# Kernel tuning notes

Measured on AMD Instinct MI355X. Metric: run time of the kernel, lower is better.

## Reference

```python
import jax, jax.numpy as jnp
import numpy as np

BETA = 0.25
SK_EPSILONS = [0.0, 0.0, 0.003]
SK_ITERS = 50
B_SIZE = 262144
LATENT_DIM = 32
K = 256


def setup_inputs() -> dict:
    key = jax.random.key(0)
    kz, k0, k1, k2 = jax.random.split(key, 4)
    return {
        "z": jax.random.normal(kz, (B_SIZE, LATENT_DIM), dtype=jnp.float32),
        "cb0": jax.random.normal(k0, (K, LATENT_DIM), dtype=jnp.float32),
        "cb1": jax.random.normal(k1, (K, LATENT_DIM), dtype=jnp.float32),
        "cb2": jax.random.normal(k2, (K, LATENT_DIM), dtype=jnp.float32),
    }


def _sq_dists(residual, codebook):
    # ||r - c||^2 = ||r||^2 + ||c||^2 - 2 r.c  -> (B, K), avoids (B,K,D) broadcast
    r2 = jnp.sum(residual * residual, axis=1, keepdims=True)      # (B,1)
    c2 = jnp.sum(codebook * codebook, axis=1)                     # (K,)
    cross = residual @ codebook.T                                 # (B,K)
    return r2 + c2 - 2.0 * cross


def _sinkhorn(d_centered, epsilon, n_iters):
    # log-domain Sinkhorn-Knopp, matches torch reference
    B, Kk = d_centered.shape
    log_B = jnp.log(jnp.asarray(B, dtype=d_centered.dtype))
    log_K = jnp.log(jnp.asarray(Kk, dtype=d_centered.dtype))
    log_Q = -d_centered / epsilon
    log_Q = log_Q - jax.scipy.special.logsumexp(log_Q)

    def body(_, lq):
        lq = lq - jax.scipy.special.logsumexp(lq, axis=1, keepdims=True) - log_B
        lq = lq - jax.scipy.special.logsumexp(lq, axis=0, keepdims=True) - log_K
        return lq

    log_Q = jax.lax.fori_loop(0, n_iters, body, log_Q)
    return jnp.exp(log_Q + log_B)


def _quantize_level(residual, codebook, sk_epsilon, use_sk=True):
    dists = _sq_dists(residual, codebook)  # (B, K)
    codes_argmin = jnp.argmin(dists, axis=-1)
    if use_sk and sk_epsilon > 0:
        d = jax.lax.stop_gradient(dists)
        d_max = jnp.max(d)
        d_min = jnp.min(d)
        mid = (d_max + d_min) / 2
        amp = jnp.maximum(d_max - mid, 1e-05)
        Q = _sinkhorn((d - mid) / amp, sk_epsilon, SK_ITERS)
        bad = jnp.any(jnp.isnan(Q)) | jnp.any(jnp.isinf(Q))
        codes = jnp.where(bad, codes_argmin, jnp.argmax(Q, axis=-1))
    else:
        codes = codes_argmin
    quantized = codebook[codes]  # (B, D) gather
    return codes, quantized


def reference(z, cb0, cb1, cb2):
    codebooks = [cb0, cb1, cb2]
    sg = jax.lax.stop_gradient
    residual = z
    all_codes = []
    quantized_total = jnp.zeros_like(z)
    rq_loss = jnp.asarray(0.0, dtype=z.dtype)
    for codebook, sk_epsilon in zip(codebooks, SK_EPSILONS):
        codes, e = _quantize_level(residual, codebook, sk_epsilon, use_sk=True)
        all_codes.append(codes)
        rq_loss = rq_loss + jnp.mean((sg(residual) - e) ** 2)
        rq_loss = rq_loss + BETA * jnp.mean((residual - sg(e)) ** 2)
        e_st = residual + sg(e - residual)  # straight-through
        quantized_total = quantized_total + e_st
        residual = residual - sg(e)
    return (all_codes[0], all_codes[1], all_codes[2], quantized_total, rq_loss)
```

## Files before the change

### kernel.cpp

```cpp
#include <hip/hip_runtime.h>


#define BSZ   262144
#define DIM   32
#define KK    256
#define CHUNK 128
#define NBLK  (BSZ / CHUNK)
#define NIBLK (BSZ / 256)
#define LROW  36
#define SKEPS 0.003f
#define NIT   50

#define WS_SSQ  0
#define WS_MINK 1
#define WS_MAXK 2
#define WS_TWOT 3
#define WS_W0   256
#define WS_WA   512
#define WS_C2   1024
#define WSB_SIG 8192
#define WSB_BH  32768
#define WSB_BL  49152
#define WSB_QB  65536

#define OC0   0
#define OC1   BSZ
#define OC2   (2 * BSZ)
#define OQ    (3 * BSZ)
#define OLOSS (3 * BSZ + BSZ * DIM)
#define OU_AH (3u * BSZ)
#define OU_AL (3u * BSZ + 4194304u)

typedef short short8 __attribute__((ext_vector_type(8)));
typedef _Float16 half8 __attribute__((ext_vector_type(8)));
typedef float f32x4 __attribute__((ext_vector_type(4)));

#if __has_builtin(__builtin_amdgcn_exp2f)
#define EXP2(x) __builtin_amdgcn_exp2f(x)
#else
#define EXP2(x) exp2f(x)
#endif

#if __has_builtin(__builtin_amdgcn_update_dpp)
#define ROR16(x, N)                                                            \
  __int_as_float(__builtin_amdgcn_update_dpp(__float_as_int(x),                \
                 __float_as_int(x), 0x120 + (N), 0xF, 0xF, false))
#define ROR16I(x, N) __builtin_amdgcn_update_dpp((x), (x), 0x120 + (N), 0xF, 0xF, false)
#else
#define ROR16(x, N) __shfl_xor((x), (N))
#define ROR16I(x, N) __shfl_xor((x), (N))
#endif

__device__ __forceinline__ float wred_sum(float x) {
  x += ROR16(x, 1); x += ROR16(x, 2); x += ROR16(x, 4); x += ROR16(x, 8);
  x += __shfl_xor(x, 16); x += __shfl_xor(x, 32);
  return x;
}
__device__ __forceinline__ float wred_max(float x) {
  x = fmaxf(x, ROR16(x, 1)); x = fmaxf(x, ROR16(x, 2));
  x = fmaxf(x, ROR16(x, 4)); x = fmaxf(x, ROR16(x, 8));
  x = fmaxf(x, __shfl_xor(x, 16)); x = fmaxf(x, __shfl_xor(x, 32));
  return x;
}
__device__ __forceinline__ float wred_min(float x) {
  x = fminf(x, ROR16(x, 1)); x = fminf(x, ROR16(x, 2));
  x = fminf(x, ROR16(x, 4)); x = fminf(x, ROR16(x, 8));
  x = fminf(x, __shfl_xor(x, 16)); x = fminf(x, __shfl_xor(x, 32));
  return x;
}
__device__ __forceinline__ float g16_max(float x) {
  x = fmaxf(x, ROR16(x, 1)); x = fmaxf(x, ROR16(x, 2));
  x = fmaxf(x, ROR16(x, 4)); x = fmaxf(x, ROR16(x, 8));
  return x;
}
__device__ __forceinline__ float g16_sum(float x) {
  x += ROR16(x, 1); x += ROR16(x, 2); x += ROR16(x, 4); x += ROR16(x, 8);
  return x;
}
__device__ __forceinline__ void g16_argmax(float& v, int& j) {
  { float ov = ROR16(v,1); int oj = ROR16I(j,1); if (ov > v || (ov == v && oj < j)) { v = ov; j = oj; } }
  { float ov = ROR16(v,2); int oj = ROR16I(j,2); if (ov > v || (ov == v && oj < j)) { v = ov; j = oj; } }
  { float ov = ROR16(v,4); int oj = ROR16I(j,4); if (ov > v || (ov == v && oj < j)) { v = ov; j = oj; } }
  { float ov = ROR16(v,8); int oj = ROR16I(j,8); if (ov > v || (ov == v && oj < j)) { v = ov; j = oj; } }
}

__device__ __forceinline__ unsigned fkey(float f) {
  unsigned b = __float_as_uint(f);
  return (b & 0x80000000u) ? ~b : (b | 0x80000000u);
}
__device__ __forceinline__ float fkeyinv(unsigned k) {
  return __uint_as_float((k & 0x80000000u) ? (k ^ 0x80000000u) : ~k);
}
__device__ __forceinline__ unsigned pk2h(_Float16 a, _Float16 b) {
  unsigned short ua = __builtin_bit_cast(unsigned short, a);
  unsigned short ub = __builtin_bit_cast(unsigned short, b);
  return (unsigned)ua | ((unsigned)ub << 16);
}
__device__ __forceinline__ unsigned short bf16rne(float x) {
  unsigned u = __float_as_uint(x);
  return (unsigned short)((u + 0x7FFFu + ((u >> 16) & 1u)) >> 16);
}
__device__ __forceinline__ float bf2f(unsigned short h) {
  return __uint_as_float(((unsigned)h) << 16);
}
__device__ __forceinline__ void split3_8(const float* xs, short8& a1, short8& a2, short8& a3) {
#pragma unroll
  for (int u = 0; u < 8; ++u) {
    float x = xs[u];
    unsigned short b1 = bf16rne(x); x -= bf2f(b1);
    unsigned short b2 = bf16rne(x); x -= bf2f(b2);
    unsigned short b3 = bf16rne(x);
    a1[u] = (short)b1; a2[u] = (short)b2; a3[u] = (short)b3;
  }
}
__device__ __forceinline__ f32x4 mfma6r(short8 A1, short8 A2, short8 A3,
                                        short8 B1, short8 B2, short8 B3, f32x4 acc) {
  acc = __builtin_amdgcn_mfma_f32_16x16x32_bf16(A3, B1, acc, 0, 0, 0);
  acc = __builtin_amdgcn_mfma_f32_16x16x32_bf16(A1, B3, acc, 0, 0, 0);
  acc = __builtin_amdgcn_mfma_f32_16x16x32_bf16(A2, B2, acc, 0, 0, 0);
  acc = __builtin_amdgcn_mfma_f32_16x16x32_bf16(A2, B1, acc, 0, 0, 0);
  acc = __builtin_amdgcn_mfma_f32_16x16x32_bf16(A1, B2, acc, 0, 0, 0);
  acc = __builtin_amdgcn_mfma_f32_16x16x32_bf16(A1, B1, acc, 0, 0, 0);
  return acc;
}
__device__ __forceinline__ void build_a(const float* zl, int b, int lane,
                                        short8& A1, short8& A2, short8& A3) {
  int row = b * 16 + (lane & 15);
  int kb = (lane >> 4) * 8;
  float xs[8];
  float4 t0 = *reinterpret_cast<const float4*>(&zl[row * LROW + kb]);
  float4 t1 = *reinterpret_cast<const float4*>(&zl[row * LROW + kb + 4]);
  xs[0]=t0.x; xs[1]=t0.y; xs[2]=t0.z; xs[3]=t0.w;
  xs[4]=t1.x; xs[5]=t1.y; xs[6]=t1.z; xs[7]=t1.w;
  split3_8(xs, A1, A2, A3);
}

__global__ void prep0_k(const float* __restrict__ cb0, const float* __restrict__ cb1,
                        const float* __restrict__ cb2, unsigned* __restrict__ wsu,
                        float* __restrict__ wsf, uint4* __restrict__ qb,
                        unsigned long long* __restrict__ sig) {
  int t = threadIdx.x;
#pragma unroll
  for (int i = 0; i < 12; ++i) sig[i * 256 + t] = 0ull;
  if (t == 0) { wsu[WS_SSQ] = 0u; wsu[WS_MINK] = 0xFFFFFFFFu; wsu[WS_MAXK] = 0u; }
  const float* cbs[3] = {cb0, cb1, cb2};
  for (int lvl = 0; lvl < 3; ++lvl) {
    const float* cb = cbs[lvl];
    float s = 0.f;
#pragma unroll
    for (int d = 0; d < DIM; ++d) { float c = cb[t * DIM + d]; s = fmaf(c, c, s); }
    wsf[WS_C2 + lvl * 256 + t] = 0.5f * s;
    for (int g = 0; g < 4; ++g) {
      int slot = g * 256 + t;
      int jt = slot >> 6, l = slot & 63;
      int col = jt * 16 + (l & 15), kb = (l >> 4) * 8;
      float xs[8];
#pragma unroll
      for (int u = 0; u < 8; ++u) xs[u] = cb[col * DIM + kb + u];
      short8 b1, b2, b3;
      split3_8(xs, b1, b2, b3);
      qb[(lvl * 3 + 0) * 1024 + slot] = __builtin_bit_cast(uint4, b1);
      qb[(lvl * 3 + 1) * 1024 + slot] = __builtin_bit_cast(uint4, b2);
      qb[(lvl * 3 + 2) * 1024 + slot] = __builtin_bit_cast(uint4, b3);
    }
  }
}

__device__ __forceinline__ void loadq(uint4* dst, const uint4* __restrict__ src, int tid) {
#pragma unroll
  for (int i = 0; i < 12; ++i) dst[i * 256 + tid] = src[i * 256 + tid];
}

__device__ __forceinline__ void argmin2_lds(const uint4* qlds, const float* cini,
                                            const float* zl, int* codel, int lane, int wid) {
  short8 A1a, A2a, A3a, A1b, A2b, A3b;
  build_a(zl, wid * 2 + 0, lane, A1a, A2a, A3a);
  build_a(zl, wid * 2 + 1, lane, A1b, A2b, A3b);
  float bva[4] = {-3.4e38f, -3.4e38f, -3.4e38f, -3.4e38f};
  float bvb[4] = {-3.4e38f, -3.4e38f, -3.4e38f, -3.4e38f};
  int bja[4] = {0, 0, 0, 0}, bjb[4] = {0, 0, 0, 0};
#pragma unroll 2
  for (int jt = 0; jt < 16; ++jt) {
    float cv = cini[jt * 16 + (lane & 15)];
    short8 B1 = __builtin_bit_cast(short8, qlds[jt * 64 + lane]);
    short8 B2 = __builtin_bit_cast(short8, qlds[1024 + jt * 64 + lane]);
    short8 B3 = __builtin_bit_cast(short8, qlds[2048 + jt * 64 + lane]);
    int col = jt * 16 + (lane & 15);
    f32x4 aa = {cv, cv, cv, cv};
    aa = mfma6r(A1a, A2a, A3a, B1, B2, B3, aa);
    f32x4 ab = {cv, cv, cv, cv};
    ab = mfma6r(A1b, A2b, A3b, B1, B2, B3, ab);
#pragma unroll
    for (int r = 0; r < 4; ++r) {
      if (aa[r] > bva[r]) { bva[r] = aa[r]; bja[r] = col; }
      if (ab[r] > bvb[r]) { bvb[r] = ab[r]; bjb[r] = col; }
    }
  }
#pragma unroll
  for (int r = 0; r < 4; ++r) g16_argmax(bva[r], bja[r]);
#pragma unroll
  for (int r = 0; r < 4; ++r) g16_argmax(bvb[r], bjb[r]);
  if ((lane & 15) == 0) {
#pragma unroll
    for (int r = 0; r < 4; ++r) {
      codel[(wid * 2 + 0) * 16 + (lane >> 4) * 4 + r] = bja[r];
      codel[(wid * 2 + 1) * 16 + (lane >> 4) * 4 + r] = bjb[r];
    }
  }
}

__device__ __forceinline__ float remap_phase(const float* __restrict__ cb, float* zl,
                                             const int* codel, int tid) {
  int row = tid & (CHUNK - 1);
  int half = tid >> 7;
  const float4* cbg = reinterpret_cast<const float4*>(cb + codel[row] * DIM + half * 16);
  float4* zr = reinterpret_cast<float4*>(&zl[row * LROW + half * 16]);
  float local = 0.f;
#pragma unroll
  for (int k = 0; k < 4; ++k) {
    float4 cv = cbg[k];
    float4 v = zr[k];
    v.x -= cv.x; v.y -= cv.y; v.z -= cv.z; v.w -= cv.w;
    zr[k] = v;
    local = fmaf(v.x, v.x, local); local = fmaf(v.y, v.y, local);
    local = fmaf(v.z, v.z, local); local = fmaf(v.w, v.w, local);
  }
  return local;
}

__global__ __launch_bounds__(256, 2) void stageA_k(const float* __restrict__ z,
                                                   const float* __restrict__ cb0,
                                                   const float* __restrict__ cb1,
                                                   float* __restrict__ out,
                                                   unsigned* __restrict__ outu,
                                                   unsigned* __restrict__ wsu,
                                                   float* __restrict__ wsf,
                                                   const uint4* __restrict__ qb) {
  __shared__ float zl[CHUNK * LROW];
  __shared__ uint4 qlds[3 * 1024];
  __shared__ float c2l[256];
  __shared__ float rsq[CHUNK];
  __shared__ int codel[CHUNK];
  __shared__ float red[4];
  const int tid = threadIdx.x, lane = tid & 63, wid = tid >> 6;
  const long base = (long)blockIdx.x * CHUNK;

#pragma unroll
  for (int g = 0; g < 4; ++g) {
    int f4 = g * 256 + tid;
    float4 v = reinterpret_cast<const float4*>(z + base * DIM)[f4];
    int row = f4 >> 3, d = (f4 & 7) * 4;
    *reinterpret_cast<float4*>(&zl[row * LROW + d]) = v;
  }
  loadq(qlds, qb, tid);
  c2l[tid] = -wsf[WS_C2 + tid];
  __syncthreads();

  float loss_acc = 0.f;

  argmin2_lds(qlds, c2l, zl, codel, lane, wid);
  __syncthreads();
  if (tid < CHUNK) out[OC0 + base + tid] = (float)codel[tid];
  loss_acc += remap_phase(cb0, zl, codel, tid);
  loadq(qlds, qb + 3 * 1024, tid);
  c2l[tid] = -wsf[WS_C2 + 256 + tid];
  __syncthreads();

  argmin2_lds(qlds, c2l, zl, codel, lane, wid);
  __syncthreads();
  if (tid < CHUNK) out[OC1 + base + tid] = (float)codel[tid];
  loss_acc += remap_phase(cb1, zl, codel, tid);
  loadq(qlds, qb + 6 * 1024, tid);
  c2l[tid] = -wsf[WS_C2 + 512 + tid];
  __syncthreads();

  if (tid < CHUNK) {
    float s = 0.f;
#pragma unroll
    for (int d = 0; d < DIM; ++d) { float x = zl[tid * LROW + d]; s = fmaf(x, x, s); }
    rsq[tid] = s;
  }
  __syncthreads();

  {
    short8 A1a, A2a, A3a, A1b, A2b, A3b;
    build_a(zl, wid * 2 + 0, lane, A1a, A2a, A3a);
    build_a(zl, wid * 2 + 1, lane, A1b, A2b, A3b);
    float mna[4] = {3.4e38f, 3.4e38f, 3.4e38f, 3.4e38f};
    float mxa[4] = {-3.4e38f, -3.4e38f, -3.4e38f, -3.4e38f};
    float mnb[4] = {3.4e38f, 3.4e38f, 3.4e38f, 3.4e38f};
    float mxb[4] = {-3.4e38f, -3.4e38f, -3.4e38f, -3.4e38f};
#pragma unroll 2
    for (int jt = 0; jt < 16; ++jt) {
      float cv = c2l[jt * 16 + (lane & 15)];
      short8 B1 = __builtin_bit_cast(short8, qlds[jt * 64 + lane]);
      short8 B2 = __builtin_bit_cast(short8, qlds[1024 + jt * 64 + lane]);
      short8 B3 = __builtin_bit_cast(short8, qlds[2048 + jt * 64 + lane]);
      f32x4 aa = {cv, cv, cv, cv};
      aa = mfma6r(A1a, A2a, A3a, B1, B2, B3, aa);
      f32x4 ab = {cv, cv, cv, cv};
      ab = mfma6r(A1b, A2b, A3b, B1, B2, B3, ab);
#pragma unroll
      for (int r = 0; r < 4; ++r) {
        mna[r] = fminf(mna[r], aa[r]); mxa[r] = fmaxf(mxa[r], aa[r]);
        mnb[r] = fminf(mnb[r], ab[r]); mxb[r] = fmaxf(mxb[r], ab[r]);
      }
    }
    float dmn = 3.4e38f, dmx = -3.4e38f;
#pragma unroll
    for (int r = 0; r < 4; ++r) {
      float r2a = rsq[(wid * 2 + 0) * 16 + (lane >> 4) * 4 + r];
      float r2b = rsq[(wid * 2 + 1) * 16 + (lane >> 4) * 4 + r];
      dmn = fminf(dmn, fminf(fmaf(-2.f, mxa[r], r2a), fmaf(-2.f, mxb[r], r2b)));
      dmx = fmaxf(dmx, fmaxf(fmaf(-2.f, mna[r], r2a), fmaf(-2.f, mnb[r], r2b)));
    }
    dmn = wred_min(dmn);
    dmx = wred_max(dmx);
    if (lane == 0) {
      atomicMin(&wsu[WS_MINK], fkey(dmn));
      atomicMax(&wsu[WS_MAXK], fkey(dmx));
    }
  }

#pragma unroll
  for (int g2 = 0; g2 < 8; ++g2) {
    int slot = g2 * 256 + tid;
    int b = slot >> 8;
    int l = (slot >> 2) & 63;
    int u = slot & 3;
    int row = b * 16 + (l & 15);
    int k = (l >> 4) * 8 + u * 2;
    float x0 = zl[row * LROW + k], x1 = zl[row * LROW + k + 1];
    _Float16 h0 = (_Float16)x0, h1 = (_Float16)x1;
    _Float16 q0 = (_Float16)(x0 - (float)h0), q1 = (_Float16)(x1 - (float)h1);
    unsigned gbase = ((unsigned)blockIdx.x * 8u + (unsigned)b) * 256u + (unsigned)(l * 4 + u);
    outu[OU_AH + gbase] = pk2h(h0, h1);
    outu[OU_AL + gbase] = pk2h(q0, q1);
  }

  loss_acc = wred_sum(loss_acc);
  if (lane == 0) red[wid] = loss_acc;
  __syncthreads();
  if (tid == 0) atomicAdd(&wsf[WS_SSQ], red[0] + red[1] + red[2] + red[3]);
}

__global__ void prep_k(const float* __restrict__ cb2, unsigned* __restrict__ wsu,
                       float* __restrict__ wsf, unsigned* __restrict__ bh,
                       unsigned* __restrict__ bl, uint4* __restrict__ qb) {
  int j = threadIdx.x;
  float dmin = fkeyinv(wsu[WS_MINK]);
  float dmax = fkeyinv(wsu[WS_MAXK]);
  float mid = (dmax + dmin) * 0.5f;
  float amp = fmaxf(dmax - mid, 1e-5f);
  float t = 1.0f / (amp * SKEPS);
  const float L2E = 1.4426950408889634f;
  float T2L = 2.0f * t * L2E;
  if (j == 0) wsf[WS_TWOT] = T2L;
  float s = 0.f;
#pragma unroll
  for (int d = 0; d < DIM; ++d) { float c = cb2[j * DIM + d]; s = fmaf(c, c, s); }
  wsf[WS_W0 + j] = -t * L2E * s;
  for (int g = 0; g < 16; ++g) {
    int slot = g * 256 + j;
    int jt = slot >> 8, l = (slot >> 2) & 63, u = slot & 3;
    int col = jt * 16 + (l & 15);
    int k = (l >> 4) * 8 + u * 2;
    float b0 = T2L * cb2[col * DIM + k], b1 = T2L * cb2[col * DIM + k + 1];
    _Float16 h0 = (_Float16)b0, h1 = (_Float16)b1;
    _Float16 q0 = (_Float16)(b0 - (float)h0), q1 = (_Float16)(b1 - (float)h1);
    bh[slot] = pk2h(h0, h1);
    bl[slot] = pk2h(q0, q1);
  }
  for (int g = 0; g < 4; ++g) {
    int slot = g * 256 + j;
    int jt = slot >> 6, l = slot & 63;
    int col = jt * 16 + (l & 15), kb = (l >> 4) * 8;
    float xs[8];
#pragma unroll
    for (int u = 0; u < 8; ++u) xs[u] = T2L * cb2[col * DIM + kb + u];
    short8 b1v, b2v, b3v;
    split3_8(xs, b1v, b2v, b3v);
    qb[9 * 1024 + slot]  = __builtin_bit_cast(uint4, b1v);
    qb[10 * 1024 + slot] = __builtin_bit_cast(uint4, b2v);
    qb[11 * 1024 + slot] = __builtin_bit_cast(uint4, b3v);
  }
}

__global__ __launch_bounds__(256, 4) void iter_k(const uint4* __restrict__ afh,
                                                 const uint4* __restrict__ afl,
                                                 const uint4* __restrict__ bfh,
                                                 const uint4* __restrict__ bfl,
                                                 const float* __restrict__ w_rd,
                                                 float* __restrict__ w_wr,
                                                 const unsigned long long* __restrict__ s_rd,
                                                 unsigned long long* __restrict__ s_wr,
                                                 unsigned long long* __restrict__ s_zr,
                                                 int first) {
  __shared__ uint4 Blo[1024];
  __shared__ float wsh[KK];
  __shared__ float exm[8][2][2][16];
  __shared__ float exs[8][2][2][16];
  __shared__ float ssh[2][KK];
  const int tid = threadIdx.x, lane = tid & 63, wv = tid >> 6;
  const int pair = wv >> 1, ch = wv & 1, g = lane >> 4;

  {
    unsigned long long tt = s_rd[tid] + s_rd[256 + tid] + s_rd[512 + tid] + s_rd[768 + tid];
    float wj = first ? w_rd[tid]
                     : w_rd[tid] + 34.0f - log2f(fmaxf((float)tt, 1.0f));
    wsh[tid] = wj;
    if (blockIdx.x == 0) {
      w_wr[tid] = wj;
      s_zr[tid] = 0ull; s_zr[256 + tid] = 0ull;
      s_zr[512 + tid] = 0ull; s_zr[768 + tid] = 0ull;
    }
  }
#pragma unroll
  for (int i = 0; i < 4; ++i) Blo[i * 256 + tid] = bfl[i * 256 + tid];
  half8 Bh[8];
#pragma unroll
  for (int jt = 0; jt < 8; ++jt)
    Bh[jt] = __builtin_bit_cast(half8, bfh[(ch * 8 + jt) * 64 + lane]);
  __syncthreads();
  float wc[8];
#pragma unroll
  for (int c = 0; c < 8; ++c) wc[c] = wsh[(ch * 8 + c) * 16 + (lane & 15)];

  float sg[8] = {0.f, 0.f, 0.f, 0.f, 0.f, 0.f, 0.f, 0.f};

#pragma unroll 1
  for (int b = 0; b < 8; ++b) {
    const int batchid = blockIdx.x * 16 + pair * 8 + b;
    half8 Ah = __builtin_bit_cast(half8, afh[batchid * 64 + lane]);
    half8 Al = __builtin_bit_cast(half8, afl[batchid * 64 + lane]);
    f32x4 v[8];
#pragma unroll
    for (int jt = 0; jt < 8; ++jt) {
      half8 Blv = __builtin_bit_cast(half8, Blo[(ch * 8 + jt) * 64 + lane]);
      f32x4 acc = {wc[jt], wc[jt], wc[jt], wc[jt]};
      acc = __builtin_amdgcn_mfma_f32_16x16x32_f16(Al, Bh[jt], acc, 0, 0, 0);
      acc = __builtin_amdgcn_mfma_f32_16x16x32_f16(Ah, Blv, acc, 0, 0, 0);
      acc = __builtin_amdgcn_mfma_f32_16x16x32_f16(Ah, Bh[jt], acc, 0, 0, 0);
      v[jt] = acc;
    }
    float m[4];
#pragma unroll
    for (int r = 0; r < 4; ++r) {
      float a01 = fmaxf(v[0][r], v[1][r]), a23 = fmaxf(v[2][r], v[3][r]);
      float a45 = fmaxf(v[4][r], v[5][r]), a67 = fmaxf(v[6][r], v[7][r]);
      m[r] = g16_max(fmaxf(fmaxf(a01, a23), fmaxf(a45, a67)));
    }
    float s[4];
#pragma unroll
    for (int r = 0; r < 4; ++r) {
#pragma unroll
      for (int jt = 0; jt < 8; ++jt) v[jt][r] = EXP2(v[jt][r] - m[r]);
      float s01 = v[0][r] + v[1][r], s23 = v[2][r] + v[3][r];
      float s45 = v[4][r] + v[5][r], s67 = v[6][r] + v[7][r];
      s[r] = g16_sum((s01 + s23) + (s45 + s67));
    }
    if ((lane & 15) == 0) {
      *reinterpret_cast<float4*>(&exm[b][pair][ch][g * 4]) = make_float4(m[0], m[1], m[2], m[3]);
      *reinterpret_cast<float4*>(&exs[b][pair][ch][g * 4]) = make_float4(s[0], s[1], s[2], s[3]);
    }
    __syncthreads();
    float4 pm = *reinterpret_cast<const float4*>(&exm[b][pair][ch ^ 1][g * 4]);
    float4 ps = *reinterpret_cast<const float4*>(&exs[b][pair][ch ^ 1][g * 4]);
    float rinv[4];
    {
      float pmv[4] = {pm.x, pm.y, pm.z, pm.w};
      float psv[4] = {ps.x, ps.y, ps.z, ps.w};
#pragma unroll
      for (int r = 0; r < 4; ++r) {
        float M = fmaxf(m[r], pmv[r]);
        float sc = EXP2(m[r] - M);
        float tot = fmaf(s[r], sc, psv[r] * EXP2(pmv[r] - M));
        rinv[r] = sc * __builtin_amdgcn_rcpf(tot);
      }
    }
#pragma unroll
    for (int jt = 0; jt < 8; ++jt)
#pragma unroll
      for (int r = 0; r < 4; ++r) sg[jt] = fmaf(v[jt][r], rinv[r], sg[jt]);
  }
#pragma unroll
  for (int jt = 0; jt < 8; ++jt) {
    float x = sg[jt];
    x += __shfl_xor(x, 16); x += __shfl_xor(x, 32);
    sg[jt] = x;
  }
  if (lane < 16) {
#pragma unroll
    for (int jt = 0; jt < 8; ++jt) ssh[pair][ch * 128 + jt * 16 + lane] = sg[jt];
  }
  __syncthreads();
  float stot = ssh[0][tid] + ssh[1][tid];
  atomicAdd(s_wr + (blockIdx.x & 3) * 256 + tid,
            (unsigned long long)fmaf(stot, 16777216.0f, 0.5f));
}

__global__ __launch_bounds__(256, 2) void fcodes_k(const float* __restrict__ z,
                                                   const float* __restrict__ cb0,
                                                   const float* __restrict__ cb1,
                                                   float* __restrict__ out,
                                                   const uint4* __restrict__ qb,
                                                   const float* __restrict__ w_rd,
                                                   const unsigned long long* __restrict__ s_rd) {
  __shared__ float zl[CHUNK * LROW];
  __shared__ uint4 qlds[3 * 1024];
  __shared__ float wsh[KK];
  __shared__ int codel[CHUNK];
  const int tid = threadIdx.x, lane = tid & 63, wid = tid >> 6;
  const long base = (long)blockIdx.x * CHUNK;

  {
    unsigned long long tt = s_rd[tid] + s_rd[256 + tid] + s_rd[512 + tid] + s_rd[768 + tid];
    wsh[tid] = w_rd[tid] + 34.0f - log2f(fmaxf((float)tt, 1.0f));
  }
  loadq(qlds, qb + 9 * 1024, tid);
#pragma unroll
  for (int g = 0; g < 4; ++g) {
    int f4 = g * 256 + tid;
    float4 v = reinterpret_cast<const float4*>(z + base * DIM)[f4];
    int row = f4 >> 3, d = (f4 & 7) * 4;
    *reinterpret_cast<float4*>(&zl[row * LROW + d]) = v;
  }
  __syncthreads();
  {
    int row = tid & (CHUNK - 1);
    int half = tid >> 7;
    int c0 = (int)out[OC0 + base + row];
    int c1 = (int)out[OC1 + base + row];
    const float4* e0 = reinterpret_cast<const float4*>(cb0 + c0 * DIM + half * 16);
    const float4* e1 = reinterpret_cast<const float4*>(cb1 + c1 * DIM + half * 16);
    float4* zr = reinterpret_cast<float4*>(&zl[row * LROW + half * 16]);
#pragma unroll
    for (int k = 0; k < 4; ++k) {
      float4 a = e0[k], bb = e1[k], v = zr[k];
      v.x = (v.x - a.x) - bb.x; v.y = (v.y - a.y) - bb.y;
      v.z = (v.z - a.z) - bb.z; v.w = (v.w - a.w) - bb.w;
      zr[k] = v;
    }
  }
  __syncthreads();

  argmin2_lds(qlds, wsh, zl, codel, lane, wid);
  __syncthreads();
  if (tid < CHUNK) out[OC2 + base + tid] = (float)codel[tid];
}

__global__ __launch_bounds__(256) void fout_k(const float* __restrict__ z,
                                              const float* __restrict__ cb0,
                                              const float* __restrict__ cb1,
                                              const float* __restrict__ cb2,
                                              float* __restrict__ out,
                                              float* __restrict__ wsf) {
  __shared__ int cc0[256], cc1[256], cc2[256];
  __shared__ float red[4];
  const int tid = threadIdx.x, lane = tid & 63, wv = tid >> 6;
  const long rbase = (long)blockIdx.x * 256;
  cc0[tid] = (int)out[OC0 + rbase + tid];
  cc1[tid] = (int)out[OC1 + rbase + tid];
  cc2[tid] = (int)out[OC2 + rbase + tid];
  __syncthreads();
  float loss = 0.f;
#pragma unroll
  for (int g = 0; g < 8; ++g) {
    long f4 = (long)blockIdx.x * 2048 + g * 256 + tid;
    int lrow = (g * 256 + tid) >> 3;
    int d4 = (g * 256 + tid) & 7;
    float4 zv = reinterpret_cast<const float4*>(z)[f4];
    float4 e0 = *reinterpret_cast<const float4*>(&cb0[cc0[lrow] * DIM + d4 * 4]);
    float4 e1 = *reinterpret_cast<const float4*>(&cb1[cc1[lrow] * DIM + d4 * 4]);
    float4 e2 = *reinterpret_cast<const float4*>(&cb2[cc2[lrow] * DIM + d4 * 4]);
    float4 q;
    q.x = (e0.x + e1.x) + e2.x; q.y = (e0.y + e1.y) + e2.y;
    q.z = (e0.z + e1.z) + e2.z; q.w = (e0.w + e1.w) + e2.w;
    reinterpret_cast<float4*>(out + OQ)[f4] = q;
    float rx = ((zv.x - e0.x) - e1.x) - e2.x;
    float ry = ((zv.y - e0.y) - e1.y) - e2.y;
    float rz = ((zv.z - e0.z) - e1.z) - e2.z;
    float rw = ((zv.w - e0.w) - e1.w) - e2.w;
    loss = fmaf(rx, rx, loss); loss = fmaf(ry, ry, loss);
    loss = fmaf(rz, rz, loss); loss = fmaf(rw, rw, loss);
  }
  loss = wred_sum(loss);
  if (lane == 0) red[wv] = loss;
  __syncthreads();
  if (tid == 0) atomicAdd(&wsf[WS_SSQ], red[0] + red[1] + red[2] + red[3]);
}

__global__ void losswrite_k(float* __restrict__ out, const float* __restrict__ wsf) {
  if (threadIdx.x == 0) out[OLOSS] = 1.25f * wsf[WS_SSQ] / 8388608.0f;
}

extern "C" void kernel_launch(void* const* d_in, const int* in_sizes, int n_in,
                              void* d_out, int out_size, void* d_ws, size_t ws_size,
                              hipStream_t stream) {
  const float* z   = (const float*)d_in[0];
  const float* cb0 = (const float*)d_in[1];
  const float* cb1 = (const float*)d_in[2];
  const float* cb2 = (const float*)d_in[3];
  float* out = (float*)d_out;
  unsigned* outu = (unsigned*)d_out;
  float* wsf = (float*)d_ws;
  unsigned* wsu = (unsigned*)d_ws;
  unsigned long long* sig = (unsigned long long*)((char*)d_ws + WSB_SIG);
  unsigned* bh = (unsigned*)((char*)d_ws + WSB_BH);
  unsigned* bl = (unsigned*)((char*)d_ws + WSB_BL);
  uint4* qb = (uint4*)((char*)d_ws + WSB_QB);

  const uint4* afh = (const uint4*)(outu + OU_AH);
  const uint4* afl = (const uint4*)(outu + OU_AL);
  const uint4* bfh = (const uint4*)bh;
  const uint4* bfl = (const uint4*)bl;

  prep0_k<<<1, 256, 0, stream>>>(cb0, cb1, cb2, wsu, wsf, qb, sig);
  stageA_k<<<NBLK, 256, 0, stream>>>(z, cb0, cb1, out, outu, wsu, wsf, qb);
  prep_k<<<1, 256, 0, stream>>>(cb2, wsu, wsf, bh, bl, qb);
  for (int it = 0; it < NIT; ++it) {
    const float* w_rd = (it == 0) ? (wsf + WS_W0) : (wsf + WS_WA + ((it - 1) & 1) * KK);
    float* w_wr = wsf + WS_WA + (it & 1) * KK;
    const unsigned long long* s_rd = sig + 1024 * ((it + 2) % 3);
    unsigned long long* s_wr = sig + 1024 * (it % 3);
    unsigned long long* s_zr = sig + 1024 * ((it + 1) % 3);
    iter_k<<<NIBLK, 256, 0, stream>>>(afh, afl, bfh, bfl, w_rd, w_wr, s_rd, s_wr, s_zr,
                                      it == 0 ? 1 : 0);
  }
  fcodes_k<<<NBLK, 256, 0, stream>>>(z, cb0, cb1, out, qb,
                                     wsf + WS_WA + ((NIT - 1) & 1) * KK,
                                     sig + 1024 * ((NIT - 1) % 3));
  fout_k<<<NIBLK, 256, 0, stream>>>(z, cb0, cb1, cb2, out, wsf);
  losswrite_k<<<1, 64, 0, stream>>>(out, wsf);
}
```

Baseline: 1.981 ms.

## Give each wave all 256 columns per row tile, dropping cross-wave softmax exchange

Each wave in the Sinkhorn iteration kernel now computes all 16 column tiles for its own 4 row batches, so the row logsumexp is finished inside the wave. This removes the per-batch LDS exchange of partial max/sum between wave pairs and the __syncthreads it needed. Both hi and lo codebook fragments now live in LDS instead of the hi half sitting in registers, and launch bounds drop occupancy from 4 to 3 blocks because more accumulators are live. The cost is extra LDS reads per MFMA and higher register pressure.

```diff
diff --git a/kernel.cpp b/kernel.cpp
--- a/kernel.cpp
+++ b/kernel.cpp
@@ -386,7 +386,7 @@
   }
 }
 
-__global__ __launch_bounds__(256, 4) void iter_k(const uint4* __restrict__ afh,
+__global__ __launch_bounds__(256, 3) void iter_k(const uint4* __restrict__ afh,
                                                  const uint4* __restrict__ afl,
                                                  const uint4* __restrict__ bfh,
                                                  const uint4* __restrict__ bfl,
@@ -396,13 +396,10 @@
                                                  unsigned long long* __restrict__ s_wr,
                                                  unsigned long long* __restrict__ s_zr,
                                                  int first) {
-  __shared__ uint4 Blo[1024];
+  __shared__ uint4 Blds[2048];
   __shared__ float wsh[KK];
-  __shared__ float exm[8][2][2][16];
-  __shared__ float exs[8][2][2][16];
-  __shared__ float ssh[2][KK];
+  __shared__ float ssh[4][KK];
   const int tid = threadIdx.x, lane = tid & 63, wv = tid >> 6;
-  const int pair = wv >> 1, ch = wv & 1, g = lane >> 4;
 
   {
     unsigned long long tt = s_rd[tid] + s_rd[256 + tid] + s_rd[512 + tid] + s_rd[768 + tid];
@@ -416,87 +413,65 @@
     }
   }
 #pragma unroll
-  for (int i = 0; i < 4; ++i) Blo[i * 256 + tid] = bfl[i * 256 + tid];
-  half8 Bh[8];
-#pragma unroll
-  for (int jt = 0; jt < 8; ++jt)
-    Bh[jt] = __builtin_bit_cast(half8, bfh[(ch * 8 + jt) * 64 + lane]);
-  __syncthreads();
-  float wc[8];
-#pragma unroll
-  for (int c = 0; c < 8; ++c) wc[c] = wsh[(ch * 8 + c) * 16 + (lane & 15)];
-
-  float sg[8] = {0.f, 0.f, 0.f, 0.f, 0.f, 0.f, 0.f, 0.f};
+  for (int i = 0; i < 4; ++i) Blds[i * 256 + tid] = bfh[i * 256 + tid];
+#pragma unroll
+  for (int i = 0; i < 4; ++i) Blds[1024 + i * 256 + tid] = bfl[i * 256 + tid];
+  __syncthreads();
+
+  float sg[16];
+#pragma unroll
+  for (int jt = 0; jt < 16; ++jt) sg[jt] = 0.f;
 
 #pragma unroll 1
-  for (int b = 0; b < 8; ++b) {
-    const int batchid = blockIdx.x * 16 + pair * 8 + b;
+  for (int b = 0; b < 4; ++b) {
+    const int batchid = blockIdx.x * 16 + wv * 4 + b;
     half8 Ah = __builtin_bit_cast(half8, afh[batchid * 64 + lane]);
     half8 Al = __builtin_bit_cast(half8, afl[batchid * 64 + lane]);
-    f32x4 v[8];
-#pragma unroll
-    for (int jt = 0; jt < 8; ++jt) {
-      half8 Blv = __builtin_bit_cast(half8, Blo[(ch * 8 + jt) * 64 + lane]);
-      f32x4 acc = {wc[jt], wc[jt], wc[jt], wc[jt]};
-      acc = __builtin_amdgcn_mfma_f32_16x16x32_f16(Al, Bh[jt], acc, 0, 0, 0);
-      acc = __builtin_amdgcn_mfma_f32_16x16x32_f16(Ah, Blv, acc, 0, 0, 0);
-      acc = __builtin_amdgcn_mfma_f32_16x16x32_f16(Ah, Bh[jt], acc, 0, 0, 0);
-      v[jt] = acc;
-    }
-    float m[4];
+    f32x4 p[16];
+#pragma unroll
+    for (int jt = 0; jt < 16; ++jt) {
+      half8 Bh = __builtin_bit_cast(half8, Blds[jt * 64 + lane]);
+      half8 Bl = __builtin_bit_cast(half8, Blds[1024 + jt * 64 + lane]);
+      float wcv = wsh[jt * 16 + (lane & 15)];
+      f32x4 acc = {wcv, wcv, wcv, wcv};
+      acc = __builtin_amdgcn_mfma_f32_16x16x32_f16(Al, Bh, acc, 0, 0, 0);
+      acc = __builtin_amdgcn_mfma_f32_16x16x32_f16(Ah, Bl, acc, 0, 0, 0);
+      acc = __builtin_amdgcn_mfma_f32_16x16x32_f16(Ah, Bh, acc, 0, 0, 0);
+      p[jt] = acc;
+    }
 #pragma unroll
     for (int r = 0; r < 4; ++r) {
-      float a01 = fmaxf(v[0][r], v[1][r]), a23 = fmaxf(v[2][r], v[3][r]);
-      float a45 = fmaxf(v[4][r], v[5][r]), a67 = fmaxf(v[6][r], v[7][r]);
-      m[r] = g16_max(fmaxf(fmaxf(a01, a23), fmaxf(a45, a67)));
-    }
-    float s[4];
-#pragma unroll
-    for (int r = 0; r < 4; ++r) {
-#pragma unroll
-      for (int jt = 0; jt < 8; ++jt) v[jt][r] = EXP2(v[jt][r] - m[r]);
-      float s01 = v[0][r] + v[1][r], s23 = v[2][r] + v[3][r];
-      float s45 = v[4][r] + v[5][r], s67 = v[6][r] + v[7][r];
-      s[r] = g16_sum((s01 + s23) + (s45 + s67));
-    }
-    if ((lane & 15) == 0) {
-      *reinterpret_cast<float4*>(&exm[b][pair][ch][g * 4]) = make_float4(m[0], m[1], m[2], m[3]);
-      *reinterpret_cast<float4*>(&exs[b][pair][ch][g * 4]) = make_float4(s[0], s[1], s[2], s[3]);
-    }
-    __syncthreads();
-    float4 pm = *reinterpret_cast<const float4*>(&exm[b][pair][ch ^ 1][g * 4]);
-    float4 ps = *reinterpret_cast<const float4*>(&exs[b][pair][ch ^ 1][g * 4]);
-    float rinv[4];
-    {
-      float pmv[4] = {pm.x, pm.y, pm.z, pm.w};
-      float psv[4] = {ps.x, ps.y, ps.z, ps.w};
-#pragma unroll
-      for (int r = 0; r < 4; ++r) {
-        float M = fmaxf(m[r], pmv[r]);
-        float sc = EXP2(m[r] - M);
-        float tot = fmaf(s[r], sc, psv[r] * EXP2(pmv[r] - M));
-        rinv[r] = sc * __builtin_amdgcn_rcpf(tot);
-      }
-    }
-#pragma unroll
-    for (int jt = 0; jt < 8; ++jt)
-#pragma unroll
-      for (int r = 0; r < 4; ++r) sg[jt] = fmaf(v[jt][r], rinv[r], sg[jt]);
-  }
-#pragma unroll
-  for (int jt = 0; jt < 8; ++jt) {
+      float a0 = fmaxf(fmaxf(p[0][r], p[1][r]), fmaxf(p[2][r], p[3][r]));
+      float a1 = fmaxf(fmaxf(p[4][r], p[5][r]), fmaxf(p[6][r], p[7][r]));
+      float a2 = fmaxf(fmaxf(p[8][r], p[9][r]), fmaxf(p[10][r], p[11][r]));
+      float a3 = fmaxf(fmaxf(p[12][r], p[13][r]), fmaxf(p[14][r], p[15][r]));
+      float m = g16_max(fmaxf(fmaxf(a0, a1), fmaxf(a2, a3)));
+#pragma unroll
+      for (int jt = 0; jt < 16; ++jt) p[jt][r] = EXP2(p[jt][r] - m);
+      float s0 = (p[0][r] + p[1][r]) + (p[2][r] + p[3][r]);
+      float s1 = (p[4][r] + p[5][r]) + (p[6][r] + p[7][r]);
+      float s2 = (p[8][r] + p[9][r]) + (p[10][r] + p[11][r]);
+      float s3 = (p[12][r] + p[13][r]) + (p[14][r] + p[15][r]);
+      float s = g16_sum((s0 + s1) + (s2 + s3));
+      float ri = __builtin_amdgcn_rcpf(s);
+#pragma unroll
+      for (int jt = 0; jt < 16; ++jt) sg[jt] = fmaf(p[jt][r], ri, sg[jt]);
+    }
+  }
+#pragma unroll
+  for (int jt = 0; jt < 16; ++jt) {
     float x = sg[jt];
     x += __shfl_xor(x, 16); x += __shfl_xor(x, 32);
     sg[jt] = x;
   }
   if (lane < 16) {
 #pragma unroll
-    for (int jt = 0; jt < 8; ++jt) ssh[pair][ch * 128 + jt * 16 + lane] = sg[jt];
-  }
-  __syncthreads();
-  float stot = ssh[0][tid] + ssh[1][tid];
+    for (int jt = 0; jt < 16; ++jt) ssh[wv][jt * 16 + lane] = sg[jt];
+  }
+  __syncthreads();
+  float scol = ssh[0][tid] + ssh[1][tid] + ssh[2][tid] + ssh[3][tid];
   atomicAdd(s_wr + (blockIdx.x & 3) * 256 + tid,
-            (unsigned long long)fmaf(stot, 16777216.0f, 0.5f));
+            (unsigned long long)fmaf(scol, 16777216.0f, 0.5f));
 }
 
 __global__ __launch_bounds__(256, 2) void fcodes_k(const float* __restrict__ z,
```

Result: slower. 7.634 ms (+285.4%).
